# Kernel tuning notes

Measured on AMD Instinct MI355X. Metric: run time of the kernel, lower is better.

## Reference

```python
import jax, jax.numpy as jnp
import numpy as np

N = 1024
DIM = 128
HEADS = 8
DK = DIM // HEADS
EDIM = 16
EPS = 1e-5
NEG = -10000.0


def _lin(k, din, dout):
    return jax.random.normal(k, (din, dout), jnp.float32) * (1.0 / np.sqrt(din))


def setup_inputs() -> dict:
    key = jax.random.key(0)
    ks = jax.random.split(key, 10)
    mask = jax.random.randint(ks[2], (N, N), 0, 2).astype(bool)
    mask = mask | jnp.eye(N, dtype=bool)  # self-loops always valid
    return {
        "x": jax.random.normal(ks[0], (N, DIM), jnp.float32),
        "edge_feat": jax.random.normal(ks[1], (N, N, EDIM), jnp.float32),
        "mask": mask,
        "Wq": _lin(ks[3], DIM, DIM), "bq": jnp.zeros((DIM,), jnp.float32),
        "Wk": _lin(ks[4], DIM, DIM), "bk": jnp.zeros((DIM,), jnp.float32),
        "Wv": _lin(ks[5], DIM, DIM), "bv": jnp.zeros((DIM,), jnp.float32),
        "Wae": _lin(ks[6], EDIM, HEADS), "bae": jnp.zeros((HEADS,), jnp.float32),
        "Wve": _lin(ks[7], EDIM, DIM), "bve": jnp.zeros((DIM,), jnp.float32),
        "Wo": _lin(ks[8], DIM, DIM), "bo": jnp.zeros((DIM,), jnp.float32),
        "gamma": jnp.ones((DIM,), jnp.float32),
        "beta": jnp.zeros((DIM,), jnp.float32),
    }


def reference(x, edge_feat, mask, Wq, bq, Wk, bk, Wv, bv, Wae, bae, Wve, bve, Wo, bo, gamma, beta):
    n, dim = x.shape
    heads = bae.shape[0]
    dk = dim // heads
    # pre-LayerNorm
    mu = jnp.mean(x, axis=-1, keepdims=True)
    var = jnp.mean(jnp.square(x - mu), axis=-1, keepdims=True)
    h = (x - mu) * jax.lax.rsqrt(var + EPS) * gamma + beta
    q = (h @ Wq + bq).reshape(n, heads, dk)
    k = (h @ Wk + bk).reshape(n, heads, dk)
    v = (h @ Wv + bv).reshape(n, heads, dk)
    # attention logits with per-edge additive bias: (n, m, heads)
    att = jnp.einsum('nhd,mhd->nmh', q, k) / np.sqrt(dk).astype(np.float32)
    att = att + edge_feat @ Wae + bae
    att = jnp.where(mask[..., None], att, NEG)
    alpha = jax.nn.softmax(att, axis=1)  # softmax over source nodes m
    # edge-conditioned values: msg_{nm} = v_m + U(e_{nm})
    edge_val = (edge_feat @ Wve + bve).reshape(n, n, heads, dk)
    out = jnp.einsum('nmh,mhd->nhd', alpha, v) + jnp.einsum('nmh,nmhd->nhd', alpha, edge_val)
    out = out.reshape(n, dim) @ Wo + bo
    return x + out
```

## Files before the change

kernel.cpp:

```cpp
#include <hip/hip_runtime.h>
#include <hip/hip_bf16.h>

#define NNODE 1024
#define DIM 128
#define HEADS 8
#define DK 16
#define EDIM 16
#define BN 8
#define NGRP 8
#define LOG2E 1.44269504f

#define PAR 768
#define WREG (2 * PAR)
#define SMEM_F 8448

__global__ __launch_bounds__(384)
void ln_qkv_kernel(const float* __restrict__ x,
                   const float* __restrict__ Wq, const float* __restrict__ bq,
                   const float* __restrict__ Wk, const float* __restrict__ bk,
                   const float* __restrict__ Wv, const float* __restrict__ bv,
                   const float* __restrict__ gamma, const float* __restrict__ beta,
                   const int* __restrict__ mask,
                   float* __restrict__ qg, float* __restrict__ kg, float* __restrict__ vg,
                   unsigned char* __restrict__ maskb) {
    const int n = blockIdx.x;
    const int t = threadIdx.x;
    __shared__ float hrow[DIM];
    __shared__ float part[4];

    if (t < 128) {
        const int* mrow = mask + (size_t)n * NNODE + t * 8;
        unsigned pb = 0;
        #pragma unroll
        for (int i = 0; i < 8; ++i) pb |= (mrow[i] ? 1u : 0u) << i;
        maskb[(size_t)n * 128 + t] = (unsigned char)pb;
    }

    float xv = 0.f;
    if (t < 128) {
        xv = x[n * DIM + t];
        float v = xv;
        #pragma unroll
        for (int off = 32; off >= 1; off >>= 1) v += __shfl_xor(v, off);
        if ((t & 63) == 0) part[t >> 6] = v;
    }
    __syncthreads();
    const float mu = (part[0] + part[1]) * (1.0f / DIM);
    const float dx = xv - mu;
    if (t < 128) {
        float v = dx * dx;
        #pragma unroll
        for (int off = 32; off >= 1; off >>= 1) v += __shfl_xor(v, off);
        if ((t & 63) == 0) part[2 + (t >> 6)] = v;
    }
    __syncthreads();
    if (t < 128) {
        const float var = (part[2] + part[3]) * (1.0f / DIM);
        hrow[t] = dx * rsqrtf(var + 1e-5f) * gamma[t] + beta[t];
    }
    __syncthreads();

    const int which = t >> 7;
    const int col = t & 127;
    const float* W = (which == 0) ? Wq : (which == 1) ? Wk : Wv;
    const float* b = (which == 0) ? bq : (which == 1) ? bk : bv;
    float* o       = (which == 0) ? qg : (which == 1) ? kg : vg;
    float a0 = b[col], a1 = 0.f;
    #pragma unroll 8
    for (int i = 0; i < DIM; i += 2) {
        a0 = fmaf(hrow[i],     W[i * DIM + col],       a0);
        a1 = fmaf(hrow[i + 1], W[(i + 1) * DIM + col], a1);
    }
    o[n * DIM + col] = a0 + a1;
}

__device__ __forceinline__ void gll16(const float* g, float* l) {
    auto* gp = (const __attribute__((address_space(1))) unsigned int*)(g);
    auto* lp = (__attribute__((address_space(3))) unsigned int*)(l);
    __builtin_amdgcn_global_load_lds(gp, lp, 16, 0, 0);
}

__global__ __launch_bounds__(256, 2)
void attn_kernel(const float* __restrict__ qg, const float* __restrict__ kg,
                 const float* __restrict__ vg, const float* __restrict__ ef,
                 const unsigned char* __restrict__ maskb,
                 const float* __restrict__ Wae, const float* __restrict__ bae,
                 float* __restrict__ acc) {
    const int t = threadIdx.x;
    const int lane = t & 63;
    const int wid = t >> 6;
    const int sp = lane >> 5;
    const int np = (lane >> 3) & 3;
    const int h  = lane & 7;
    const int bx = blockIdx.x;
    const int n0  = (bx >> 3) * BN;
    const int grp = bx & 7;
    const int mb_w = grp * 128 + wid * 32;

    __shared__ float smem[SMEM_F];
    float* wreg = smem + wid * WREG;

    float qreg[2][DK];
    #pragma unroll
    for (int hf = 0; hf < 2; ++hf) {
        const float* qp = qg + (size_t)(n0 + np + 4 * hf) * DIM + h * DK;
        #pragma unroll
        for (int d4 = 0; d4 < 4; ++d4) {
            const float4 qv = *(const float4*)(qp + d4 * 4);
            qreg[hf][d4 * 4 + 0] = qv.x; qreg[hf][d4 * 4 + 1] = qv.y;
            qreg[hf][d4 * 4 + 2] = qv.z; qreg[hf][d4 * 4 + 3] = qv.w;
        }
    }
    float waec[EDIM];
    #pragma unroll
    for (int e = 0; e < EDIM; ++e) waec[e] = Wae[e * HEADS + h] * LOG2E;
    const float baeh = bae[h] * LOG2E;

    unsigned mk0 = *(const unsigned*)(maskb + (size_t)(n0 + np)     * 128 + (mb_w >> 3)) >> sp;
    unsigned mk1 = *(const unsigned*)(maskb + (size_t)(n0 + np + 4) * 128 + (mb_w >> 3)) >> sp;

    float sl[2] = {0.f, 0.f};
    float accv[2][DK], accT[2][EDIM];
    #pragma unroll
    for (int hf = 0; hf < 2; ++hf) {
        #pragma unroll
        for (int d = 0; d < DK; ++d) accv[hf][d] = 0.f;
        #pragma unroll
        for (int e = 0; e < EDIM; ++e) accT[hf][e] = 0.f;
    }

    const int s0   = lane & 3;
    const int h0   = (lane >> 2) & 7;
    const int row0 = lane >> 5;
    const int koffl = row0 * 128 + h0 * 16 + (((s0 - (h0 >> 1)) & 3) << 2);
    const int nn0 = lane >> 3;
    const int mm0 = (lane >> 2) & 1;
    const int eoffl = nn0 * (NNODE * EDIM) + mm0 * EDIM + (((s0 - nn0) & 3) << 2);
    const float* efb = ef + (size_t)n0 * NNODE * EDIM;

    int krot[4], erot[4];
    const int rotk = (h >> 1) & 3;
    #pragma unroll
    for (int i = 0; i < 4; ++i) {
        krot[i] = ((i + rotk) & 3) << 2;
        erot[i] = ((i + np) & 3) << 2;
    }

#define ISSUE_BATCH(DB, MB)                                              \
    do {                                                                 \
        float* db = (DB);                                                \
        gll16(kg + (size_t)(MB) * DIM + koffl, db);                      \
        gll16(vg + (size_t)(MB) * DIM + koffl, db + 256);                \
        gll16(efb + (size_t)(MB) * EDIM + eoffl, db + 512);              \
    } while (0)

#define COMPUTE_CHUNK(DB)                                                      \
    do {                                                                       \
        const float* kl = (DB) + sp * 128 + h * 16;                            \
        const float* vl = kl + 256;                                            \
        const float* eb = (DB) + 512 + np * 32 + sp * 16;                      \
        float kk[DK], vv[DK];                                                  \
        _Pragma("unroll")                                                      \
        for (int i = 0; i < 4; ++i) {                                          \
            const float4 k4 = *(const float4*)(kl + krot[i]);                  \
            kk[i*4+0]=k4.x; kk[i*4+1]=k4.y; kk[i*4+2]=k4.z; kk[i*4+3]=k4.w;    \
            const float4 v4 = *(const float4*)(vl + krot[i]);                  \
            vv[i*4+0]=v4.x; vv[i*4+1]=v4.y; vv[i*4+2]=v4.z; vv[i*4+3]=v4.w;    \
        }                                                                      \
        _Pragma("unroll")                                                      \
        for (int hf = 0; hf < 2; ++hf) {                                       \
            float efv[EDIM];                                                   \
            _Pragma("unroll")                                                  \
            for (int i = 0; i < 4; ++i) {                                      \
                const float4 e4 = *(const float4*)(eb + hf * 128 + erot[i]);   \
                efv[i*4+0]=e4.x; efv[i*4+1]=e4.y;                              \
                efv[i*4+2]=e4.z; efv[i*4+3]=e4.w;                              \
            }                                                                  \
            float bias = baeh, dot = 0.f;                                      \
            _Pragma("unroll")                                                  \
            for (int e = 0; e < EDIM; ++e) bias = fmaf(efv[e], waec[e], bias); \
            _Pragma("unroll")                                                  \
            for (int d = 0; d < DK; ++d) dot = fmaf(qreg[hf][d], kk[d], dot);  \
            const float lg = fmaf(dot, 0.25f * LOG2E, bias);                   \
            const unsigned mv = (hf ? mk1 : mk0) & 1u;                         \
            const float p = mv ? __builtin_amdgcn_exp2f(lg) : 0.f;             \
            sl[hf] += p;                                                       \
            _Pragma("unroll")                                                  \
            for (int d = 0; d < DK; ++d) accv[hf][d] = fmaf(p, vv[d], accv[hf][d]); \
            _Pragma("unroll")                                                  \
            for (int e = 0; e < EDIM; ++e) accT[hf][e] = fmaf(p, efv[e], accT[hf][e]); \
        }                                                                      \
        mk0 >>= 2; mk1 >>= 2;                                                  \
    } while (0)

    ISSUE_BATCH(wreg, mb_w);

    #pragma unroll 1
    for (int cc = 0; cc < 16; cc += 2) {
        ISSUE_BATCH(wreg + PAR, mb_w + 2 * (cc + 1));
        asm volatile("s_waitcnt vmcnt(3)" ::: "memory");
        COMPUTE_CHUNK(wreg);
        if (cc < 14) {
            ISSUE_BATCH(wreg, mb_w + 2 * (cc + 2));
            asm volatile("s_waitcnt vmcnt(3)" ::: "memory");
        } else {
            asm volatile("s_waitcnt vmcnt(0)" ::: "memory");
        }
        COMPUTE_CHUNK(wreg + PAR);
    }
#undef ISSUE_BATCH
#undef COMPUTE_CHUNK

    #pragma unroll
    for (int hf = 0; hf < 2; ++hf) {
        sl[hf] += __shfl_xor(sl[hf], 32);
        #pragma unroll
        for (int d = 0; d < DK; ++d) accv[hf][d] += __shfl_xor(accv[hf][d], 32);
        #pragma unroll
        for (int e = 0; e < EDIM; ++e) accT[hf][e] += __shfl_xor(accT[hf][e], 32);
    }
    __syncthreads();
    float* red = smem;
    if (lane < 32) {
        float* rp = &red[((wid * 4 + np) * 8 + h) * 66];
        #pragma unroll
        for (int hf = 0; hf < 2; ++hf) {
            rp[hf * 33 + 0] = sl[hf];
            #pragma unroll
            for (int d = 0; d < DK; ++d) rp[hf * 33 + 1 + d] = accv[hf][d];
            #pragma unroll
            for (int e = 0; e < EDIM; ++e) rp[hf * 33 + 17 + e] = accT[hf][e];
        }
    }
    __syncthreads();
    for (int v = t; v < BN * HEADS * 33; v += 256) {
        const int n = v / 264;
        const int rem = v - n * 264;
        const int hh = rem / 33;
        const int idx = rem - hh * 33;
        const int nnp = n & 3, hf = n >> 2;
        float sum = 0.f;
        #pragma unroll
        for (int w = 0; w < 4; ++w)
            sum += red[((w * 4 + nnp) * 8 + hh) * 66 + hf * 33 + idx];
        acc[((size_t)(n0 + n) * NGRP + grp) * 264 + rem] = sum;
    }
}

__global__ __launch_bounds__(128)
void final_kernel(const float* __restrict__ acc,
                  const float* __restrict__ Wve, const float* __restrict__ bve,
                  const float* __restrict__ x,
                  const float* __restrict__ Wo, const float* __restrict__ bo,
                  float* __restrict__ out) {
    const int n = blockIdx.x, t = threadIdx.x;
    __shared__ float ab[HEADS * 33];
    __shared__ float orow[DIM];
    const float* ap = acc + (size_t)n * NGRP * 264;
    for (int u = t; u < HEADS * 33; u += 128) {
        float sv = 0.f;
        #pragma unroll
        for (int g = 0; g < NGRP; ++g) sv += ap[g * 264 + u];
        ab[u] = sv;
    }
    __syncthreads();
    const int col = t, hh = col >> 4, dd = col & 15;
    const float slv = ab[hh * 33];
    float acc2 = 0.f;
    #pragma unroll
    for (int e = 0; e < EDIM; ++e) acc2 = fmaf(ab[hh * 33 + 17 + e], Wve[e * DIM + col], acc2);
    orow[col] = (ab[hh * 33 + 1 + dd] + acc2) / slv + bve[col];
    __syncthreads();
    float o0 = bo[col] + x[(size_t)n * DIM + col], o1 = 0.f;
    #pragma unroll 8
    for (int i = 0; i < DIM; i += 2) {
        o0 = fmaf(orow[i],     Wo[i * DIM + col],       o0);
        o1 = fmaf(orow[i + 1], Wo[(i + 1) * DIM + col], o1);
    }
    out[(size_t)n * DIM + col] = o0 + o1;
}

extern "C" void kernel_launch(void* const* d_in, const int* in_sizes, int n_in,
                              void* d_out, int out_size, void* d_ws, size_t ws_size,
                              hipStream_t stream) {
    const float* x     = (const float*)d_in[0];
    const float* ef    = (const float*)d_in[1];
    const int*   mask  = (const int*)d_in[2];
    const float* Wq    = (const float*)d_in[3];
    const float* bq    = (const float*)d_in[4];
    const float* Wk    = (const float*)d_in[5];
    const float* bk    = (const float*)d_in[6];
    const float* Wv    = (const float*)d_in[7];
    const float* bv    = (const float*)d_in[8];
    const float* Wae   = (const float*)d_in[9];
    const float* bae   = (const float*)d_in[10];
    const float* Wve   = (const float*)d_in[11];
    const float* bve   = (const float*)d_in[12];
    const float* Wo    = (const float*)d_in[13];
    const float* bo    = (const float*)d_in[14];
    const float* gamma = (const float*)d_in[15];
    const float* beta  = (const float*)d_in[16];

    float* ws = (float*)d_ws;
    float* accb = ws;
    float* qg   = ws + (size_t)NNODE * NGRP * 264;
    float* kg   = qg + (size_t)NNODE * DIM;
    float* vg   = kg + (size_t)NNODE * DIM;
    unsigned char* maskb = (unsigned char*)(vg + (size_t)NNODE * DIM);

    ln_qkv_kernel<<<NNODE, 384, 0, stream>>>(x, Wq, bq, Wk, bk, Wv, bv, gamma, beta,
                                             mask, qg, kg, vg, maskb);
    attn_kernel<<<(NNODE / BN) * NGRP, 256, 0, stream>>>(qg, kg, vg, ef, maskb, Wae, bae, accb);
    final_kernel<<<NNODE, 128, 0, stream>>>(accb, Wve, bve, x, Wo, bo, (float*)d_out);
}
```

Baseline: 171.4 us.

## Triple-buffer async global-to-LDS loads, raise compute priority, split FMA chains

Moves the per-wave global-to-LDS prefetch of K, V and edge-feature chunks from two buffers to three, so two batches stay in flight while one is computed, with vmcnt waits adjusted to match. Compute sections are wrapped in s_setprio to favour math issue. The bias and q·k dot-product reductions are split into two independent accumulator chains to shorten dependency latency. Shared memory per block grows with the extra buffer, which may reduce occupancy.

```diff
diff --git a/kernel.cpp b/kernel.cpp
--- a/kernel.cpp
+++ b/kernel.cpp
@@ -11,8 +11,8 @@
 #define LOG2E 1.44269504f
 
 #define PAR 768
-#define WREG (2 * PAR)
-#define SMEM_F 8448
+#define WREG (3 * PAR)
+#define SMEM_F (4 * WREG)
 
 __global__ __launch_bounds__(384)
 void ln_qkv_kernel(const float* __restrict__ x,
@@ -146,16 +146,18 @@
         erot[i] = ((i + np) & 3) << 2;
     }
 
-#define ISSUE_BATCH(DB, MB)                                              \
+#define ISSUE_BATCH(DB, CH)                                              \
     do {                                                                 \
         float* db = (DB);                                                \
-        gll16(kg + (size_t)(MB) * DIM + koffl, db);                      \
-        gll16(vg + (size_t)(MB) * DIM + koffl, db + 256);                \
-        gll16(efb + (size_t)(MB) * EDIM + eoffl, db + 512);              \
+        const int mrow = mb_w + 2 * (CH);                                \
+        gll16(kg + (size_t)mrow * DIM + koffl, db);                      \
+        gll16(vg + (size_t)mrow * DIM + koffl, db + 256);                \
+        gll16(efb + (size_t)mrow * EDIM + eoffl, db + 512);              \
     } while (0)
 
 #define COMPUTE_CHUNK(DB)                                                      \
     do {                                                                       \
+        __builtin_amdgcn_s_setprio(1);                                         \
         const float* kl = (DB) + sp * 128 + h * 16;                            \
         const float* vl = kl + 256;                                            \
         const float* eb = (DB) + 512 + np * 32 + sp * 16;                      \
@@ -176,12 +178,18 @@
                 efv[i*4+0]=e4.x; efv[i*4+1]=e4.y;                              \
                 efv[i*4+2]=e4.z; efv[i*4+3]=e4.w;                              \
             }                                                                  \
-            float bias = baeh, dot = 0.f;                                      \
-            _Pragma("unroll")                                                  \
-            for (int e = 0; e < EDIM; ++e) bias = fmaf(efv[e], waec[e], bias); \
-            _Pragma("unroll")                                                  \
-            for (int d = 0; d < DK; ++d) dot = fmaf(qreg[hf][d], kk[d], dot);  \
-            const float lg = fmaf(dot, 0.25f * LOG2E, bias);                   \
+            float b0_ = baeh, b1_ = 0.f, d0_ = 0.f, d1_ = 0.f;                 \
+            _Pragma("unroll")                                                  \
+            for (int e = 0; e < EDIM; e += 2) {                                \
+                b0_ = fmaf(efv[e],     waec[e],     b0_);                      \
+                b1_ = fmaf(efv[e + 1], waec[e + 1], b1_);                      \
+            }                                                                  \
+            _Pragma("unroll")                                                  \
+            for (int d = 0; d < DK; d += 2) {                                  \
+                d0_ = fmaf(qreg[hf][d],     kk[d],     d0_);                   \
+                d1_ = fmaf(qreg[hf][d + 1], kk[d + 1], d1_);                   \
+            }                                                                  \
+            const float lg = fmaf(d0_ + d1_, 0.25f * LOG2E, b0_ + b1_);        \
             const unsigned mv = (hf ? mk1 : mk0) & 1u;                         \
             const float p = mv ? __builtin_amdgcn_exp2f(lg) : 0.f;             \
             sl[hf] += p;                                                       \
@@ -191,23 +199,34 @@
             for (int e = 0; e < EDIM; ++e) accT[hf][e] = fmaf(p, efv[e], accT[hf][e]); \
         }                                                                      \
         mk0 >>= 2; mk1 >>= 2;                                                  \
+        __builtin_amdgcn_s_setprio(0);                                         \
     } while (0)
 
-    ISSUE_BATCH(wreg, mb_w);
+    ISSUE_BATCH(wreg, 0);
+    ISSUE_BATCH(wreg + PAR, 1);
 
     #pragma unroll 1
-    for (int cc = 0; cc < 16; cc += 2) {
-        ISSUE_BATCH(wreg + PAR, mb_w + 2 * (cc + 1));
-        asm volatile("s_waitcnt vmcnt(3)" ::: "memory");
+    for (int cc = 0; cc < 12; cc += 3) {
+        ISSUE_BATCH(wreg + 2 * PAR, cc + 2);
+        asm volatile("s_waitcnt vmcnt(6)" ::: "memory");
         COMPUTE_CHUNK(wreg);
-        if (cc < 14) {
-            ISSUE_BATCH(wreg, mb_w + 2 * (cc + 2));
-            asm volatile("s_waitcnt vmcnt(3)" ::: "memory");
-        } else {
-            asm volatile("s_waitcnt vmcnt(0)" ::: "memory");
-        }
+        ISSUE_BATCH(wreg, cc + 3);
+        asm volatile("s_waitcnt vmcnt(6)" ::: "memory");
         COMPUTE_CHUNK(wreg + PAR);
-    }
+        ISSUE_BATCH(wreg + PAR, cc + 4);
+        asm volatile("s_waitcnt vmcnt(6)" ::: "memory");
+        COMPUTE_CHUNK(wreg + 2 * PAR);
+    }
+    ISSUE_BATCH(wreg + 2 * PAR, 14);
+    asm volatile("s_waitcnt vmcnt(6)" ::: "memory");
+    COMPUTE_CHUNK(wreg);
+    ISSUE_BATCH(wreg, 15);
+    asm volatile("s_waitcnt vmcnt(6)" ::: "memory");
+    COMPUTE_CHUNK(wreg + PAR);
+    asm volatile("s_waitcnt vmcnt(3)" ::: "memory");
+    COMPUTE_CHUNK(wreg + 2 * PAR);
+    asm volatile("s_waitcnt vmcnt(0)" ::: "memory");
+    COMPUTE_CHUNK(wreg);
 #undef ISSUE_BATCH
 #undef COMPUTE_CHUNK
 
```

Result: slower. 300.2 us (+75.1%).

## Deepen edge-feature prefetch to four buffers, decoupled from K/V double buffer

Applied to the files above, without the earlier changes.

Splits the per-chunk global-to-LDS load batch into a K/V part (double-buffered) and an edge-feature part (quad-buffered), so edge features are fetched two chunks ahead while K/V stay one chunk ahead. The loop is unrolled by four with explicit vmcnt waits and an epilogue. The aim is to hide the latency of the large edge-feature stream, which dominates traffic. It costs more LDS per wave, which may reduce occupancy, and the hand-written waitcnt accounting must stay correct.

```diff
diff --git a/kernel.cpp b/kernel.cpp
--- a/kernel.cpp
+++ b/kernel.cpp
@@ -10,8 +10,7 @@
 #define NGRP 8
 #define LOG2E 1.44269504f
 
-#define PAR 768
-#define WREG (2 * PAR)
+#define WREG 2048
 #define SMEM_F 8448
 
 __global__ __launch_bounds__(384)
@@ -146,19 +145,24 @@
         erot[i] = ((i + np) & 3) << 2;
     }
 
-#define ISSUE_BATCH(DB, MB)                                              \
+#define KVB(p) (wreg + (p) * 512)
+#define EFB(b) (wreg + 1024 + (b) * 256)
+
+#define ISSUE_KV(DB, CH)                                                 \
     do {                                                                 \
-        float* db = (DB);                                                \
-        gll16(kg + (size_t)(MB) * DIM + koffl, db);                      \
-        gll16(vg + (size_t)(MB) * DIM + koffl, db + 256);                \
-        gll16(efb + (size_t)(MB) * EDIM + eoffl, db + 512);              \
+        const int mrow = mb_w + 2 * (CH);                                \
+        gll16(kg + (size_t)mrow * DIM + koffl, (DB));                    \
+        gll16(vg + (size_t)mrow * DIM + koffl, (DB) + 256);              \
     } while (0)
 
-#define COMPUTE_CHUNK(DB)                                                      \
+#define ISSUE_EF(EB, CH)                                                 \
+    gll16(efb + (size_t)(mb_w + 2 * (CH)) * EDIM + eoffl, (EB))
+
+#define COMPUTE_CHUNK(KV, EB)                                                  \
     do {                                                                       \
-        const float* kl = (DB) + sp * 128 + h * 16;                            \
+        const float* kl = (KV) + sp * 128 + h * 16;                            \
         const float* vl = kl + 256;                                            \
-        const float* eb = (DB) + 512 + np * 32 + sp * 16;                      \
+        const float* eb = (EB) + np * 32 + sp * 16;                            \
         float kk[DK], vv[DK];                                                  \
         _Pragma("unroll")                                                      \
         for (int i = 0; i < 4; ++i) {                                          \
@@ -193,23 +197,41 @@
         mk0 >>= 2; mk1 >>= 2;                                                  \
     } while (0)
 
-    ISSUE_BATCH(wreg, mb_w);
+    ISSUE_EF(EFB(0), 0);
+    ISSUE_KV(KVB(0), 0);
+    ISSUE_EF(EFB(1), 1);
 
     #pragma unroll 1
-    for (int cc = 0; cc < 16; cc += 2) {
-        ISSUE_BATCH(wreg + PAR, mb_w + 2 * (cc + 1));
-        asm volatile("s_waitcnt vmcnt(3)" ::: "memory");
-        COMPUTE_CHUNK(wreg);
-        if (cc < 14) {
-            ISSUE_BATCH(wreg, mb_w + 2 * (cc + 2));
-            asm volatile("s_waitcnt vmcnt(3)" ::: "memory");
-        } else {
-            asm volatile("s_waitcnt vmcnt(0)" ::: "memory");
-        }
-        COMPUTE_CHUNK(wreg + PAR);
-    }
-#undef ISSUE_BATCH
+    for (int cc = 0; cc < 12; cc += 4) {
+        ISSUE_KV(KVB(1), cc + 1); ISSUE_EF(EFB(2), cc + 2);
+        asm volatile("s_waitcnt vmcnt(4)" ::: "memory");
+        COMPUTE_CHUNK(KVB(0), EFB(0));
+        ISSUE_KV(KVB(0), cc + 2); ISSUE_EF(EFB(3), cc + 3);
+        asm volatile("s_waitcnt vmcnt(4)" ::: "memory");
+        COMPUTE_CHUNK(KVB(1), EFB(1));
+        ISSUE_KV(KVB(1), cc + 3); ISSUE_EF(EFB(0), cc + 4);
+        asm volatile("s_waitcnt vmcnt(4)" ::: "memory");
+        COMPUTE_CHUNK(KVB(0), EFB(2));
+        ISSUE_KV(KVB(0), cc + 4); ISSUE_EF(EFB(1), cc + 5);
+        asm volatile("s_waitcnt vmcnt(4)" ::: "memory");
+        COMPUTE_CHUNK(KVB(1), EFB(3));
+    }
+    ISSUE_KV(KVB(1), 13); ISSUE_EF(EFB(2), 14);
+    asm volatile("s_waitcnt vmcnt(4)" ::: "memory");
+    COMPUTE_CHUNK(KVB(0), EFB(0));
+    ISSUE_KV(KVB(0), 14); ISSUE_EF(EFB(3), 15);
+    asm volatile("s_waitcnt vmcnt(4)" ::: "memory");
+    COMPUTE_CHUNK(KVB(1), EFB(1));
+    ISSUE_KV(KVB(1), 15);
+    asm volatile("s_waitcnt vmcnt(3)" ::: "memory");
+    COMPUTE_CHUNK(KVB(0), EFB(2));
+    asm volatile("s_waitcnt vmcnt(0)" ::: "memory");
+    COMPUTE_CHUNK(KVB(1), EFB(3));
+#undef ISSUE_KV
+#undef ISSUE_EF
 #undef COMPUTE_CHUNK
+#undef KVB
+#undef EFB
 
     #pragma unroll
     for (int hf = 0; hf < 2; ++hf) {
```

New measurement: 276.3 us. 61.2% more time.

## Deepen edge-feature prefetch to two chunks ahead with quad-buffered LDS

Applied to the files above, without the earlier changes.

Restructures the async global-to-LDS pipeline so edge-feature tiles are prefetched two chunks ahead using four rotating edge buffers, while K/V stay double-buffered. Pointer increments replace recomputed addresses. The aim is to hide the latency of the large edge_feat stream, which dominates memory traffic. It uses more LDS per wave (2048 vs 1536 floats), which could lower occupancy, and the hand-written vmcnt accounting is more fragile.

```diff
diff --git a/kernel.cpp b/kernel.cpp
--- a/kernel.cpp
+++ b/kernel.cpp
@@ -10,8 +10,7 @@
 #define NGRP 8
 #define LOG2E 1.44269504f
 
-#define PAR 768
-#define WREG (2 * PAR)
+#define WREG 2048
 #define SMEM_F 8448
 
 __global__ __launch_bounds__(384)
@@ -136,7 +135,9 @@
     const int nn0 = lane >> 3;
     const int mm0 = (lane >> 2) & 1;
     const int eoffl = nn0 * (NNODE * EDIM) + mm0 * EDIM + (((s0 - nn0) & 3) << 2);
-    const float* efb = ef + (size_t)n0 * NNODE * EDIM;
+    const float* kB = kg + (size_t)mb_w * DIM + koffl;
+    const float* vB = vg + (size_t)mb_w * DIM + koffl;
+    const float* eB = ef + (size_t)n0 * NNODE * EDIM + (size_t)mb_w * EDIM + eoffl;
 
     int krot[4], erot[4];
     const int rotk = (h >> 1) & 3;
@@ -146,19 +147,14 @@
         erot[i] = ((i + np) & 3) << 2;
     }
 
-#define ISSUE_BATCH(DB, MB)                                              \
-    do {                                                                 \
-        float* db = (DB);                                                \
-        gll16(kg + (size_t)(MB) * DIM + koffl, db);                      \
-        gll16(vg + (size_t)(MB) * DIM + koffl, db + 256);                \
-        gll16(efb + (size_t)(MB) * EDIM + eoffl, db + 512);              \
-    } while (0)
-
-#define COMPUTE_CHUNK(DB)                                                      \
+#define KVB(p) (wreg + (p) * 512)
+#define EFBUF(b) (wreg + 1024 + (b) * 256)
+
+#define COMPUTE_CHUNK(KV, EB)                                                  \
     do {                                                                       \
-        const float* kl = (DB) + sp * 128 + h * 16;                            \
+        const float* kl = (KV) + sp * 128 + h * 16;                            \
         const float* vl = kl + 256;                                            \
-        const float* eb = (DB) + 512 + np * 32 + sp * 16;                      \
+        const float* eb = (EB) + np * 32 + sp * 16;                            \
         float kk[DK], vv[DK];                                                  \
         _Pragma("unroll")                                                      \
         for (int i = 0; i < 4; ++i) {                                          \
@@ -193,23 +189,40 @@
         mk0 >>= 2; mk1 >>= 2;                                                  \
     } while (0)
 
-    ISSUE_BATCH(wreg, mb_w);
+    gll16(eB, EFBUF(0));
+    gll16(kB, KVB(0)); gll16(vB, KVB(0) + 256);
+    gll16(eB + 32, EFBUF(1));
 
     #pragma unroll 1
-    for (int cc = 0; cc < 16; cc += 2) {
-        ISSUE_BATCH(wreg + PAR, mb_w + 2 * (cc + 1));
-        asm volatile("s_waitcnt vmcnt(3)" ::: "memory");
-        COMPUTE_CHUNK(wreg);
-        if (cc < 14) {
-            ISSUE_BATCH(wreg, mb_w + 2 * (cc + 2));
-            asm volatile("s_waitcnt vmcnt(3)" ::: "memory");
-        } else {
-            asm volatile("s_waitcnt vmcnt(0)" ::: "memory");
+    for (int g = 0; g < 3; ++g) {
+        #pragma unroll
+        for (int i = 0; i < 4; ++i) {
+            float* kvN = KVB((i + 1) & 1);
+            gll16(kB + 256, kvN); gll16(vB + 256, kvN + 256);
+            gll16(eB + 64, EFBUF((i + 2) & 3));
+            asm volatile("s_waitcnt vmcnt(4)" ::: "memory");
+            COMPUTE_CHUNK(KVB(i & 1), EFBUF(i & 3));
+            kB += 256; vB += 256; eB += 32;
         }
-        COMPUTE_CHUNK(wreg + PAR);
-    }
-#undef ISSUE_BATCH
+    }
+    gll16(kB + 256, KVB(1)); gll16(vB + 256, KVB(1) + 256);
+    gll16(eB + 64, EFBUF(2));
+    asm volatile("s_waitcnt vmcnt(4)" ::: "memory");
+    COMPUTE_CHUNK(KVB(0), EFBUF(0));
+    kB += 256; vB += 256; eB += 32;
+    gll16(kB + 256, KVB(0)); gll16(vB + 256, KVB(0) + 256);
+    gll16(eB + 64, EFBUF(3));
+    asm volatile("s_waitcnt vmcnt(4)" ::: "memory");
+    COMPUTE_CHUNK(KVB(1), EFBUF(1));
+    kB += 256; vB += 256;
+    gll16(kB + 256, KVB(1)); gll16(vB + 256, KVB(1) + 256);
+    asm volatile("s_waitcnt vmcnt(3)" ::: "memory");
+    COMPUTE_CHUNK(KVB(0), EFBUF(2));
+    asm volatile("s_waitcnt vmcnt(0)" ::: "memory");
+    COMPUTE_CHUNK(KVB(1), EFBUF(3));
 #undef COMPUTE_CHUNK
+#undef KVB
+#undef EFBUF
 
     #pragma unroll
     for (int hf = 0; hf < 2; ++hf) {
```

Measured after the change: 287.3 us. +67.6%, slower.
